# Kernel optimization log

Hardware: AMD Instinct MI355X
Metric: run time of the kernel (lower is better)

The kernel has to match this reference:

```python
import jax, jax.numpy as jnp
from jax import lax
import numpy as np

# ---- model dims ----
VOCAB, DMODEL, NLAYER = 32000, 1024, 4
NHEAD, HEAD = 16, 64              # RWKV6 heads (DMODEL = NHEAD*HEAD)
DIN = 2 * DMODEL                  # mamba expand=2
MHEAD, MHD = DIN // 64, 64        # mamba heads / head_dim (hard-coded 64 in block)
DSTATE, KCONV = 64, 4             # mamba2 state size / depthwise conv kernel
FFH = 4 * DMODEL
B, T = 1, 1024
EPS = 1e-6


def rmsnorm(v, w):
    return w * v * lax.rsqrt(jnp.mean(v * v, axis=-1, keepdims=True) + EPS)


def causal_dwconv(x, w):
    # x: [B,T,C], w: [C,K] depthwise causal conv
    C, K = w.shape
    xp = jnp.pad(x, ((0, 0), (K - 1, 0), (0, 0)))
    return lax.conv_general_dilated(
        xp, w.T[:, None, :], (1,), 'VALID',
        dimension_numbers=('NWC', 'WIO', 'NWC'), feature_group_count=C)


def setup_inputs() -> dict:
    key = jax.random.key(0)
    ks = iter(jax.random.split(key, 64))
    nrm = lambda shape, s=0.02: jax.random.normal(next(ks), shape, jnp.float32) * s
    x = jax.random.randint(next(ks), (B, T), 0, VOCAB)
    inp = dict(
        x=x,
        embed=nrm((VOCAB, DMODEL)),
        ln_w=jnp.ones((NLAYER, DMODEL), jnp.float32),
        Wr=nrm((NLAYER, DMODEL, DMODEL)), Wk=nrm((NLAYER, DMODEL, DMODEL)),
        Wv=nrm((NLAYER, DMODEL, DMODEL)), Ww=nrm((NLAYER, DMODEL, DMODEL)),
        w_bias=nrm((NLAYER, DMODEL), 0.5), u=nrm((NLAYER, NHEAD, HEAD), 0.5),
        Wg=nrm((NLAYER, DMODEL, DMODEL)), Wo=nrm((NLAYER, DMODEL, DMODEL)),
        Win=nrm((NLAYER, DMODEL, 2 * DIN + 2 * DSTATE + MHEAD)),
        conv_w=nrm((NLAYER, DIN + 2 * DSTATE, KCONV), 0.2),
        dt_bias=nrm((NLAYER, MHEAD), 0.5), A_log=nrm((NLAYER, MHEAD), 0.5),
        Dskip=nrm((NLAYER, MHEAD), 0.5),
        mnorm_w=jnp.ones((NLAYER, DIN), jnp.float32),
        Wout_m=nrm((NLAYER, DIN, DMODEL)),
        gate_w=nrm((NLAYER, 2 * DMODEL)), gate_b=jnp.zeros((NLAYER,), jnp.float32),
        ffn_ln_w=jnp.ones((NLAYER, DMODEL), jnp.float32),
        W1=nrm((NLAYER, DMODEL, FFH)), W2=nrm((NLAYER, FFH, DMODEL)),
        ln_out_w=jnp.ones((DMODEL,), jnp.float32),
    )
    return inp


def _block(h, p):
    (p_ln, pWr, pWk, pWv, pWw, p_wb, p_u, pWg, pWo, pWin, p_cw, p_dtb,
     p_Al, p_D, p_mn, pWom, p_gw, p_gb, p_fln, pW1, pW2) = p
    nx = rmsnorm(h, p_ln)

    # ---- RWKV6 linear attention ----
    r = (nx @ pWr).reshape(B, T, NHEAD, HEAD)
    k = (nx @ pWk).reshape(B, T, NHEAD, HEAD)
    v = (nx @ pWv).reshape(B, T, NHEAD, HEAD)
    dec = jnp.exp(-jnp.exp(nx @ pWw + p_wb)).reshape(B, T, NHEAD, HEAD)  # data-dep decay in (0,1)
    g = jax.nn.silu(nx @ pWg)

    def rstep(S, inp):
        rt, kt, vt, dt_ = inp                      # [B,H,hd]
        kv = kt[..., None] * vt[..., None, :]      # [B,H,hd,hd]
        o = jnp.einsum('bhk,bhkv->bhv', rt, S + p_u[None, :, :, None] * kv)
        return dt_[..., None] * S + kv, o

    S0 = jnp.zeros((B, NHEAD, HEAD, HEAD), nx.dtype)
    tmaj = lambda a: jnp.moveaxis(a, 1, 0)
    _, o = lax.scan(rstep, S0, (tmaj(r), tmaj(k), tmaj(v), tmaj(dec)))
    o = jnp.moveaxis(o, 0, 1).reshape(B, T, DMODEL)
    out_rwkv = (o * g) @ pWo

    # ---- Mamba2 selective scan ----
    zxbcdt = nx @ pWin
    z = zxbcdt[..., :DIN]
    xBC = zxbcdt[..., DIN:2 * DIN + 2 * DSTATE]
    dt = zxbcdt[..., -MHEAD:]
    xBC = jax.nn.silu(causal_dwconv(xBC, p_cw))
    xm = xBC[..., :DIN].reshape(B, T, MHEAD, MHD)
    Bm = xBC[..., DIN:DIN + DSTATE]
    Cm = xBC[..., DIN + DSTATE:]
    dt = jax.nn.softplus(dt + p_dtb)               # [B,T,MH]
    dA = jnp.exp(-dt * jnp.exp(p_Al))              # [B,T,MH]

    def mstep(hst, inp):
        xt, Bt, Ct, dAt, dtt = inp                 # [B,MH,hd],[B,ds],[B,ds],[B,MH],[B,MH]
        hst = dAt[..., None, None] * hst + (dtt[..., None] * xt)[..., None] * Bt[:, None, None, :]
        y = jnp.einsum('bhps,bs->bhp', hst, Ct)
        return hst, y

    h0 = jnp.zeros((B, MHEAD, MHD, DSTATE), nx.dtype)
    _, ym = lax.scan(mstep, h0, (tmaj(xm), tmaj(Bm), tmaj(Cm), tmaj(dA), tmaj(dt)))
    ym = jnp.moveaxis(ym, 0, 1) + p_D[None, None, :, None] * xm
    ym = ym.reshape(B, T, DIN)
    ym = rmsnorm(ym * jax.nn.silu(z), p_mn)        # gated RMSNorm
    out_mamba = ym @ pWom

    # ---- gated fusion + residual + FFN ----
    cat = jnp.concatenate([out_rwkv, out_mamba], axis=-1)
    gate = jax.nn.sigmoid(jnp.einsum('btd,d->bt', cat, p_gw) + p_gb)[..., None]
    h = h + gate * out_rwkv + (1.0 - gate) * out_mamba
    h = h + jax.nn.gelu(rmsnorm(h, p_fln) @ pW1, approximate=False) @ pW2
    return h


def reference(x, embed, ln_w, Wr, Wk, Wv, Ww, w_bias, u, Wg, Wo, Win, conv_w,
              dt_bias, A_log, Dskip, mnorm_w, Wout_m, gate_w, gate_b,
              ffn_ln_w, W1, W2, ln_out_w):
    h = embed[x]  # [B,T,D]
    params = (ln_w, Wr, Wk, Wv, Ww, w_bias, u, Wg, Wo, Win, conv_w, dt_bias,
              A_log, Dskip, mnorm_w, Wout_m, gate_w, gate_b, ffn_ln_w, W1, W2)
    h, _ = lax.scan(lambda c, p: (_block(c, p), None), h, params)
    logits = rmsnorm(h, ln_out_w) @ embed.T  # tied head
    return logits
```

## Files before the change

### kernel.cpp

```cpp
#include <hip/hip_runtime.h>
#include <hip/hip_bf16.h>
#include <math.h>

#define T 1024
#define NLAYER 4
#define NHEAD 16
#define HEAD 64
#define DIN 2048
#define MHEAD 32
#define DSTATE 64
#define FFH 4096
#define NWIN 4256
#define CCONV 2176
#define VOCABSZ 32000
#define NCHUNK 16
#define PKROWS 9472
#define PKN 9376

typedef unsigned short u16;
typedef __attribute__((ext_vector_type(8))) short s16x8;
typedef __attribute__((ext_vector_type(4))) float f32x4;

__device__ inline u16 f2bf(float f) {
  union { float f; unsigned u; } v; v.f = f;
  return (u16)((v.u + 0x7FFF + ((v.u >> 16) & 1)) >> 16);
}
__device__ inline float bf2f(u16 s) {
  union { unsigned u; float f; } v; v.u = ((unsigned)s) << 16;
  return v.f;
}
__device__ inline float sigf(float x) { return 1.f / (1.f + expf(-x)); }

__device__ inline void gload16(const void* g, void* l) {
  __builtin_amdgcn_global_load_lds(
      (__attribute__((address_space(1))) void*)(size_t)g,
      (__attribute__((address_space(3))) void*)(unsigned int)(size_t)l,
      16, 0, 0);
}

#define SWZ_SRC(lane) ((((lane) & 7) ^ ((lane) >> 3)) * 8)
#define SWZ_RD(kb, lk8, rsw) (((((kb) + (lk8)) >> 3) ^ (rsw)) << 3)

__device__ inline float block_sum(float v, float* sb) {
  #pragma unroll
  for (int o = 32; o; o >>= 1) v += __shfl_down(v, o);
  int w = threadIdx.x >> 6;
  if ((threadIdx.x & 63) == 0) sb[w] = v;
  __syncthreads();
  float s = sb[0] + sb[1] + sb[2] + sb[3];
  __syncthreads();
  return s;
}

__global__ __launch_bounds__(256) void k_cast(const float* __restrict__ s, u16* __restrict__ d) {
  size_t i = ((size_t)blockIdx.x * 256 + threadIdx.x) * 4;
  float4 v = *(const float4*)&s[i];
  u16 o[4] = {f2bf(v.x), f2bf(v.y), f2bf(v.z), f2bf(v.w)};
  *(uint2*)&d[i] = *(uint2*)o;
}

__global__ __launch_bounds__(256) void k_tcast(const float* __restrict__ src, size_t sstride,
                                               u16* __restrict__ dst, size_t dstride,
                                               int K, int N) {
  __shared__ float S[64][65];
  const float* sp = src + (size_t)blockIdx.z * sstride;
  u16* dp = dst + (size_t)blockIdx.z * dstride;
  int n0 = blockIdx.x * 64, k0 = blockIdx.y * 64;
  int tid = threadIdx.x;
  int tr = tid >> 4, tc = (tid & 15) * 4;
  #pragma unroll
  for (int it = 0; it < 4; ++it) {
    int r = tr + it * 16;
    int col = n0 + tc;
    float4 v;
    if (col + 3 < N) v = *(const float4*)&sp[(size_t)(k0 + r) * N + col];
    else {
      v.x = (col + 0 < N) ? sp[(size_t)(k0 + r) * N + col + 0] : 0.f;
      v.y = (col + 1 < N) ? sp[(size_t)(k0 + r) * N + col + 1] : 0.f;
      v.z = (col + 2 < N) ? sp[(size_t)(k0 + r) * N + col + 2] : 0.f;
      v.w = 0.f;
    }
    S[r][tc + 0] = v.x; S[r][tc + 1] = v.y; S[r][tc + 2] = v.z; S[r][tc + 3] = v.w;
  }
  __syncthreads();
  #pragma unroll
  for (int it = 0; it < 4; ++it) {
    int rn = tr + it * 16;
    if (n0 + rn >= N) continue;
    u16 o[4];
    o[0] = f2bf(S[tc + 0][rn]); o[1] = f2bf(S[tc + 1][rn]);
    o[2] = f2bf(S[tc + 2][rn]); o[3] = f2bf(S[tc + 3][rn]);
    *(uint2*)&dp[(size_t)(n0 + rn) * K + k0 + tc] = *(uint2*)o;
  }
}

struct TC6 { const float* src[6]; u16* dst[6]; size_t dstride[6]; };
__global__ __launch_bounds__(256) void k_tcast6(TC6 tc) {
  __shared__ float S[64][65];
  int w = blockIdx.z >> 2, l = blockIdx.z & 3;
  const float* sp = tc.src[w] + (size_t)l * 1024 * 1024;
  u16* dp = tc.dst[w] + (size_t)l * tc.dstride[w];
  int n0 = blockIdx.x * 64, k0 = blockIdx.y * 64;
  int tid = threadIdx.x;
  int tr = tid >> 4, tcc = (tid & 15) * 4;
  #pragma unroll
  for (int it = 0; it < 4; ++it) {
    int r = tr + it * 16;
    float4 v = *(const float4*)&sp[(size_t)(k0 + r) * 1024 + n0 + tcc];
    S[r][tcc + 0] = v.x; S[r][tcc + 1] = v.y; S[r][tcc + 2] = v.z; S[r][tcc + 3] = v.w;
  }
  __syncthreads();
  #pragma unroll
  for (int it = 0; it < 4; ++it) {
    int rn = tr + it * 16;
    u16 o[4];
    o[0] = f2bf(S[tcc + 0][rn]); o[1] = f2bf(S[tcc + 1][rn]);
    o[2] = f2bf(S[tcc + 2][rn]); o[3] = f2bf(S[tcc + 3][rn]);
    *(uint2*)&dp[(size_t)(n0 + rn) * 1024 + k0 + tcc] = *(uint2*)o;
  }
}

__global__ __launch_bounds__(256) void k_embln(const int* x, const float* embed,
                                               const float* w, float* h, u16* out) {
  __shared__ float sb[8];
  int t = blockIdx.x, tid = threadIdx.x;
  int row = x[t];
  float4 v = *(const float4*)&embed[(size_t)row * 1024 + tid * 4];
  *(float4*)&h[(size_t)t * 1024 + tid * 4] = v;
  float ss = v.x * v.x + v.y * v.y + v.z * v.z + v.w * v.w;
  float tot = block_sum(ss, sb);
  float rn = rsqrtf(tot / 1024.f + 1e-6f);
  int c = tid * 4;
  u16 o[4] = {f2bf(v.x * rn * w[c + 0]), f2bf(v.y * rn * w[c + 1]),
              f2bf(v.z * rn * w[c + 2]), f2bf(v.w * rn * w[c + 3])};
  *(uint2*)&out[(size_t)t * 1024 + c] = *(uint2*)o;
}

enum { EPI_F32 = 0, EPI_QKV = 1, EPI_GELU = 2 };

struct GOut {
  void* out;
  const float* aux;
  size_t zstride;
  float *r, *k, *v, *ld, *g, *zx;
};

template <int EPI, int BM, int BN, int TH>
__global__ __launch_bounds__(TH) void k_gemm2(const u16* __restrict__ A,
                                              const u16* __restrict__ Bt,
                                              int N, int K, int kLen, GOut go) {
  union SmemG {
    u16 st[2][BM + BN][64];
    float cb[BM][BN];
  };
  __shared__ __align__(16) SmemG sm;
  constexpr int NW = TH / 64;
  constexpr int NWM = (NW == 8) ? 4 : 2;
  constexpr int NWN = NW / NWM;
  constexpr int FR = BM / NWM / 16, FC = BN / NWN / 16;
  constexpr int ROWS = BM + BN;
  constexpr int RPW = ROWS / NW;
  constexpr int LPS = RPW / 8;
  int tid = threadIdx.x, lane = tid & 63, wid = tid >> 6;
  int lid = blockIdx.y * gridDim.x + blockIdx.x;
  int nwg = gridDim.x * gridDim.y;
  int q = nwg >> 3, r8 = nwg & 7;
  int xcd = lid & 7, pos = lid >> 3;
  int wg = (xcd < r8) ? (xcd * (q + 1) + pos) : (r8 * (q + 1) + (xcd - r8) * q + pos);
  int m0 = (wg % gridDim.x) * BM, n0 = (wg / gridDim.x) * BN;
  int kOff = blockIdx.z * kLen;
  int wr = (wid / NWN) * (BM / NWM), wc = (wid % NWN) * (BN / NWN);
  int lr = lane & 15, lk8 = (lane >> 4) * 8;
  int rsw = lr & 7;
  int swc = SWZ_SRC(lane);
  int rA = lane >> 3;
  f32x4 acc[FR][FC] = {};

  auto STAGE = [&](int buf, int k0) {
    #pragma unroll
    for (int it = 0; it < LPS; ++it) {
      int rb = wid * RPW + it * 8;
      if (rb < BM)
        gload16(&A[(size_t)(m0 + rb + rA) * K + k0 + swc], &sm.st[buf][rb][0]);
      else
        gload16(&Bt[(size_t)(n0 + rb - BM + rA) * K + k0 + swc], &sm.st[buf][rb][0]);
    }
  };
  auto COMPUTE = [&](int buf) {
    #pragma unroll
    for (int kb = 0; kb < 64; kb += 32) {
      s16x8 af[FR], bf[FC];
      #pragma unroll
      for (int i = 0; i < FR; ++i)
        af[i] = *(const s16x8*)&sm.st[buf][wr + i * 16 + lr][SWZ_RD(kb, lk8, rsw)];
      #pragma unroll
      for (int j = 0; j < FC; ++j)
        bf[j] = *(const s16x8*)&sm.st[buf][BM + wc + j * 16 + lr][SWZ_RD(kb, lk8, rsw)];
      #pragma unroll
      for (int i = 0; i < FR; ++i)
        #pragma unroll
        for (int j = 0; j < FC; ++j)
          acc[i][j] = __builtin_amdgcn_mfma_f32_16x16x32_bf16(af[i], bf[j], acc[i][j], 0, 0, 0);
    }
  };

  int nt = kLen >> 6;
  STAGE(0, kOff);
  int cur = 0;
  for (int t = 0; t < nt; ++t) {
    if (t + 1 < nt) {
      STAGE(cur ^ 1, kOff + (t + 1) * 64);
      asm volatile("s_waitcnt vmcnt(%0)" :: "n"(LPS) : "memory");
    } else {
      asm volatile("s_waitcnt vmcnt(0)" ::: "memory");
    }
    __builtin_amdgcn_s_barrier();
    __builtin_amdgcn_sched_barrier(0);
    COMPUTE(cur);
    __builtin_amdgcn_s_barrier();
    cur ^= 1;
  }

  if constexpr (EPI == EPI_F32) {
    float* outf = (float*)go.out + (size_t)blockIdx.z * go.zstride;
    #pragma unroll
    for (int i = 0; i < FR; ++i)
      #pragma unroll
      for (int j = 0; j < FC; ++j) {
        int row = m0 + wr + i * 16 + ((lane >> 4) << 2);
        int col = n0 + wc + j * 16 + lr;
        if (col >= N) continue;
        #pragma unroll
        for (int r_ = 0; r_ < 4; ++r_)
          outf[(size_t)(row + r_) * N + col] = acc[i][j][r_];
      }
  } else {
    __syncthreads();
    #pragma unroll
    for (int i = 0; i < FR; ++i)
      #pragma unroll
      for (int j = 0; j < FC; ++j) {
        int rrow = wr + i * 16 + ((lane >> 4) << 2);
        int ccol = wc + j * 16 + lr;
        #pragma unroll
        for (int r_ = 0; r_ < 4; ++r_)
          sm.cb[rrow + r_][ccol] = acc[i][j][r_];
      }
    __syncthreads();
    constexpr int RPB = BN / 4;
    constexpr int ITERS = (BM * RPB) / TH;
    if constexpr (EPI == EPI_GELU) {
      u16* outb = (u16*)go.out;
      #pragma unroll
      for (int it2 = 0; it2 < ITERS; ++it2) {
        int idx = it2 * TH + tid;
        int row = idx / RPB, c4 = (idx % RPB) * 4;
        int gc = n0 + c4;
        if (gc + 3 >= N) continue;
        float4 v = *(const float4*)&sm.cb[row][c4];
        u16 o[4];
        o[0] = f2bf(0.5f * v.x * (1.f + erff(v.x * 0.70710678118654752f)));
        o[1] = f2bf(0.5f * v.y * (1.f + erff(v.y * 0.70710678118654752f)));
        o[2] = f2bf(0.5f * v.z * (1.f + erff(v.z * 0.70710678118654752f)));
        o[3] = f2bf(0.5f * v.w * (1.f + erff(v.w * 0.70710678118654752f)));
        *(uint2*)&outb[(size_t)(m0 + row) * N + gc] = *(uint2*)o;
      }
    } else {
      float* tptr; int ldbw, coff, op;
      if (n0 < 5120) {
        int tsel = n0 >> 10;
        tptr = (tsel == 0) ? go.r : (tsel == 1) ? go.k : (tsel == 2) ? go.v
             : (tsel == 3) ? go.ld : go.g;
        ldbw = 1024; coff = n0 & 1023;
        op = (tsel == 3) ? 1 : (tsel == 4) ? 2 : 0;
      } else {
        tptr = go.zx; ldbw = 4256; coff = n0 - 5120; op = 0;
      }
      #pragma unroll
      for (int it2 = 0; it2 < ITERS; ++it2) {
        int idx = it2 * TH + tid;
        int row = idx / RPB, c4 = (idx % RPB) * 4;
        int gc = n0 + c4;
        if (gc >= N) continue;
        float4 v = *(const float4*)&sm.cb[row][c4];
        float* pv = (float*)&v;
        if (op == 1) {
          #pragma unroll
          for (int e = 0; e < 4; ++e) pv[e] = -__expf(pv[e] + go.aux[coff + c4 + e]);
        } else if (op == 2) {
          #pragma unroll
          for (int e = 0; e < 4; ++e) pv[e] = pv[e] * sigf(pv[e]);
        }
        if (gc + 3 < N) *(float4*)&tptr[(size_t)(m0 + row) * ldbw + coff + c4] = v;
        else {
          for (int e = 0; e < 4 && gc + e < N; ++e)
            tptr[(size_t)(m0 + row) * ldbw + coff + c4 + e] = pv[e];
        }
      }
    }
  }
}

struct DualArg {
  const u16 *A0, *A1, *B0, *B1;
  float *o0, *o1;
  int K0, K1;
};
__global__ __launch_bounds__(256) void k_dual(DualArg da) {
  union SmemD {
    u16 st[2][128][64];
    float cb[64][64];
  };
  __shared__ __align__(16) SmemD sm;
  const u16* A  = blockIdx.z ? da.A1 : da.A0;
  const u16* Bt = blockIdx.z ? da.B1 : da.B0;
  float* out    = blockIdx.z ? da.o1 : da.o0;
  int K         = blockIdx.z ? da.K1 : da.K0;
  const int N = 1024;
  int tid = threadIdx.x, lane = tid & 63, wid = tid >> 6;
  int lid = blockIdx.y * gridDim.x + blockIdx.x;
  int nwg = gridDim.x * gridDim.y;
  int q = nwg >> 3, r8 = nwg & 7;
  int xcd = lid & 7, pos = lid >> 3;
  int wg = (xcd < r8) ? (xcd * (q + 1) + pos) : (r8 * (q + 1) + (xcd - r8) * q + pos);
  int m0 = (wg % gridDim.x) * 64, n0 = (wg / gridDim.x) * 64;
  int wr = (wid >> 1) * 32, wc = (wid & 1) * 32;
  int lr = lane & 15, lk8 = (lane >> 4) * 8;
  int rsw = lr & 7, swc = SWZ_SRC(lane), rA = lane >> 3;
  f32x4 acc[2][2] = {};
  auto STAGE = [&](int buf, int k0) {
    #pragma unroll
    for (int it = 0; it < 2; ++it) {
      int rb = wid * 16 + it * 8;
      gload16(&A[(size_t)(m0 + rb + rA) * K + k0 + swc], &sm.st[buf][rb][0]);
      gload16(&Bt[(size_t)(n0 + rb + rA) * K + k0 + swc], &sm.st[buf][64 + rb][0]);
    }
  };
  auto COMPUTE = [&](int buf) {
    #pragma unroll
    for (int kb = 0; kb < 64; kb += 32) {
      s16x8 af[2], bf[2];
      #pragma unroll
      for (int i = 0; i < 2; ++i)
        af[i] = *(const s16x8*)&sm.st[buf][wr + i * 16 + lr][SWZ_RD(kb, lk8, rsw)];
      #pragma unroll
      for (int j = 0; j < 2; ++j)
        bf[j] = *(const s16x8*)&sm.st[buf][64 + wc + j * 16 + lr][SWZ_RD(kb, lk8, rsw)];
      #pragma unroll
      for (int i = 0; i < 2; ++i)
        #pragma unroll
        for (int j = 0; j < 2; ++j)
          acc[i][j] = __builtin_amdgcn_mfma_f32_16x16x32_bf16(af[i], bf[j], acc[i][j], 0, 0, 0);
    }
  };
  int nt = K >> 6;
  STAGE(0, 0);
  int cur = 0;
  for (int t = 0; t < nt; ++t) {
    if (t + 1 < nt) {
      STAGE(cur ^ 1, (t + 1) * 64);
      asm volatile("s_waitcnt vmcnt(4)" ::: "memory");
    } else {
      asm volatile("s_waitcnt vmcnt(0)" ::: "memory");
    }
    __builtin_amdgcn_s_barrier();
    __builtin_amdgcn_sched_barrier(0);
    COMPUTE(cur);
    __builtin_amdgcn_s_barrier();
    cur ^= 1;
  }
  __syncthreads();
  #pragma unroll
  for (int i = 0; i < 2; ++i)
    #pragma unroll
    for (int j = 0; j < 2; ++j) {
      int rrow = wr + i * 16 + ((lane >> 4) << 2);
      int ccol = wc + j * 16 + lr;
      #pragma unroll
      for (int r_ = 0; r_ < 4; ++r_)
        sm.cb[rrow + r_][ccol] = acc[i][j][r_];
    }
  __syncthreads();
  #pragma unroll
  for (int it2 = 0; it2 < 4; ++it2) {
    int idx = it2 * 256 + tid;
    int row = idx >> 4, c4 = (idx & 15) * 4;
    *(float4*)&out[(size_t)(m0 + row) * N + n0 + c4] = *(const float4*)&sm.cb[row][c4];
  }
}

__global__ __launch_bounds__(256) void k_conv(const float* __restrict__ zx,
                                              const float* __restrict__ cw,
                                              float* __restrict__ xc) {
  int c = (blockIdx.x * 256 + threadIdx.x) * 4;
  int t = blockIdx.y;
  if (c >= CCONV) return;
  float4 w0 = *(const float4*)&cw[(c + 0) * 4];
  float4 w1 = *(const float4*)&cw[(c + 1) * 4];
  float4 w2 = *(const float4*)&cw[(c + 2) * 4];
  float4 w3 = *(const float4*)&cw[(c + 3) * 4];
  float4 a = {0.f, 0.f, 0.f, 0.f};
  #pragma unroll
  for (int tap = 0; tap < 4; ++tap) {
    int tt = t - 3 + tap;
    if (tt < 0) continue;
    float4 z = *(const float4*)&zx[(size_t)tt * NWIN + 2048 + c];
    a.x += z.x * ((const float*)&w0)[tap];
    a.y += z.y * ((const float*)&w1)[tap];
    a.z += z.z * ((const float*)&w2)[tap];
    a.w += z.w * ((const float*)&w3)[tap];
  }
  a.x = a.x * sigf(a.x); a.y = a.y * sigf(a.y);
  a.z = a.z * sigf(a.z); a.w = a.w * sigf(a.w);
  *(float4*)&xc[(size_t)t * CCONV + c] = a;
}

__global__ __launch_bounds__(256) void k_dtbc(const float* __restrict__ zx,
                                              const float* __restrict__ xc,
                                              const float* __restrict__ dt_bias,
                                              const float* __restrict__ A_log,
                                              float* __restrict__ dtb, float* __restrict__ la,
                                              float* __restrict__ BC) {
  int c = blockIdx.x, tid = threadIdx.x;
  if (blockIdx.y == 0) {
    __shared__ float ldaS[64][33];
    #pragma unroll
    for (int it = 0; it < 8; ++it) {
      int e = it * 256 + tid;
      int i = e >> 5, j = e & 31;
      float x = zx[(size_t)(c * 64 + i) * NWIN + 4224 + j] + dt_bias[j];
      float sp = (x > 20.f) ? x : log1pf(expf(x));
      dtb[(size_t)(c * 64 + i) * 32 + j] = sp;
      ldaS[i][j] = -sp * expf(A_log[j]);
    }
    __syncthreads();
    if (tid < 32) {
      float g = 0.f;
      for (int i = 0; i < 64; ++i) {
        g += ldaS[i][tid];
        la[((size_t)c * 32 + tid) * 64 + i] = g;
      }
    }
  } else {
    __shared__ float Bc[64][65];
    __shared__ float Cc[16][65];
    int i0 = (blockIdx.y - 1) * 16;
    #pragma unroll
    for (int it = 0; it < 4; ++it) {
      int idx = it * 256 + tid;
      int r = idx >> 4, c4 = (idx & 15) * 4;
      float4 b4 = *(const float4*)&xc[(size_t)(c * 64 + r) * CCONV + 2048 + c4];
      Bc[r][c4] = b4.x; Bc[r][c4+1] = b4.y; Bc[r][c4+2] = b4.z; Bc[r][c4+3] = b4.w;
    }
    {
      int r = tid >> 4, c4 = (tid & 15) * 4;
      float4 cv = *(const float4*)&xc[(size_t)(c * 64 + i0 + r) * CCONV + 2112 + c4];
      Cc[r][c4] = cv.x; Cc[r][c4+1] = cv.y; Cc[r][c4+2] = cv.z; Cc[r][c4+3] = cv.w;
    }
    __syncthreads();
    int il = tid >> 4, sg = tid & 15;
    float acc[4] = {};
    for (int d = 0; d < 64; ++d) {
      float cv = Cc[il][d];
      #pragma unroll
      for (int j = 0; j < 4; ++j) acc[j] += Bc[sg * 4 + j][d] * cv;
    }
    #pragma unroll
    for (int j = 0; j < 4; ++j)
      BC[((size_t)c * 64 + i0 + il) * 64 + sg * 4 + j] = acc[j];
  }
}

union SmemH1 {
  struct { float rS[64][66], kS[64][66], gS[64][66]; u16 khS[64][64]; u16 vtS[64][72]; float uS[64]; } a;
  struct { u16 XT[64][72], BT[64][72]; float fS[64]; } b;
};
__global__ __launch_bounds__(256) void k_heads1(const float* __restrict__ rbuf,
                                                const float* __restrict__ kbuf,
                                                const float* __restrict__ ldbuf,
                                                const float* __restrict__ vbuf,
                                                const float* __restrict__ u,
                                                const float* __restrict__ xc,
                                                const float* __restrict__ la,
                                                const float* __restrict__ dtb,
                                                u16* __restrict__ rt, float* __restrict__ eL,
                                                u16* __restrict__ G, float* __restrict__ U,
                                                float* __restrict__ Um) {
  __shared__ SmemH1 sm;
  int c = blockIdx.x, tid = threadIdx.x;
  int lane = tid & 63, wid = tid >> 6;
  int lr = lane & 15, lk8 = (lane >> 4) * 8, rsw = lr & 7;
  int wr = (wid >> 1) * 32, wc = (wid & 1) * 32;
  if (blockIdx.y < 16) {
    int h = blockIdx.y;
    #pragma unroll
    for (int it = 0; it < 4; ++it) {
      int idx = it * 256 + tid;
      int i = idx >> 4, c4 = (idx & 15) * 4;
      size_t base = (size_t)(c * 64 + i) * 1024 + h * 64 + c4;
      float4 rv = *(const float4*)&rbuf[base];
      float4 kv = *(const float4*)&kbuf[base];
      float4 lv = *(const float4*)&ldbuf[base];
      float4 vv = *(const float4*)&vbuf[base];
      sm.a.rS[i][c4] = rv.x; sm.a.rS[i][c4+1] = rv.y; sm.a.rS[i][c4+2] = rv.z; sm.a.rS[i][c4+3] = rv.w;
      sm.a.kS[i][c4] = kv.x; sm.a.kS[i][c4+1] = kv.y; sm.a.kS[i][c4+2] = kv.z; sm.a.kS[i][c4+3] = kv.w;
      sm.a.gS[i][c4] = lv.x; sm.a.gS[i][c4+1] = lv.y; sm.a.gS[i][c4+2] = lv.z; sm.a.gS[i][c4+3] = lv.w;
      sm.a.vtS[c4 + 0][i] = f2bf(vv.x); sm.a.vtS[c4 + 1][i] = f2bf(vv.y);
      sm.a.vtS[c4 + 2][i] = f2bf(vv.z); sm.a.vtS[c4 + 3][i] = f2bf(vv.w);
    }
    if (tid < 64) sm.a.uS[tid] = u[h * 64 + tid];
    __syncthreads();
    if (tid < 64) {
      int k = tid;
      float g = 0.f;
      for (int i = 0; i < 64; ++i) {
        float ld = sm.a.gS[i][k];
        sm.a.gS[i][k] = g;
        rt[(size_t)(c * 64 + i) * 1024 + h * 64 + k] = f2bf(sm.a.rS[i][k] * __expf(g));
        g += ld;
      }
      float gL = g;
      eL[((size_t)c * 16 + h) * 64 + k] = __expf(gL);
      for (int i = 0; i < 64; ++i) {
        float gincl = (i < 63) ? sm.a.gS[i + 1][k] : gL;
        int col = (((i >> 3) ^ (k & 7)) << 3) | (i & 7);
        sm.a.khS[k][col] = f2bf(sm.a.kS[i][k] * __expf(fminf(gL - gincl, 0.f)));
      }
    }
    __syncthreads();
    {
      int i = tid & 63, sg = tid >> 6;
      float acc[16] = {};
      float accd = 0.f;
      for (int k = 0; k < 64; ++k) {
        float rv = sm.a.rS[i][k], gi = sm.a.gS[i][k];
        accd += rv * sm.a.uS[k] * sm.a.kS[i][k];
        #pragma unroll
        for (int j = 0; j < 16; ++j) {
          int s = sg * 16 + j;
          int sp1 = (s < 63) ? s + 1 : 63;
          acc[j] += rv * sm.a.kS[s][k] * __expf(fminf(gi - sm.a.gS[sp1][k], 0.f));
        }
      }
      #pragma unroll
      for (int j = 0; j < 16; ++j) {
        int s = sg * 16 + j;
        float v = (s < i) ? acc[j] : ((s == i) ? accd : 0.f);
        G[(((size_t)c * 16 + h) * 64 + i) * 64 + s] = f2bf(v);
      }
    }
    {
      size_t gb = ((size_t)c * 16 + h) * 64;
      f32x4 acc2[2][2] = {};
      #pragma unroll
      for (int kb = 0; kb < 64; kb += 32) {
        s16x8 a[2], b[2];
        #pragma unroll
        for (int i_ = 0; i_ < 2; ++i_)
          a[i_] = *(const s16x8*)&sm.a.khS[wr + i_ * 16 + lr][SWZ_RD(kb, lk8, rsw)];
        #pragma unroll
        for (int j_ = 0; j_ < 2; ++j_)
          b[j_] = *(const s16x8*)&sm.a.vtS[wc + j_ * 16 + lr][kb + lk8];
        #pragma unroll
        for (int i_ = 0; i_ < 2; ++i_)
          #pragma unroll
          for (int j_ = 0; j_ < 2; ++j_)
            acc2[i_][j_] = __builtin_amdgcn_mfma_f32_16x16x32_bf16(a[i_], b[j_], acc2[i_][j_], 0, 0, 0);
      }
      #pragma unroll
      for (int i_ = 0; i_ < 2; ++i_)
        #pragma unroll
        for (int j_ = 0; j_ < 2; ++j_) {
          int row = wr + i_ * 16 + ((lane >> 4) << 2);
          int col = wc + j_ * 16 + lr;
          #pragma unroll
          for (int r_ = 0; r_ < 4; ++r_)
            U[(gb + row + r_) * 64 + col] = acc2[i_][j_][r_];
        }
    }
  } else {
    int h = blockIdx.y - 16;
    size_t lb = ((size_t)c * 32 + h) * 64;
    if (tid < 64) {
      float la63 = la[lb + 63];
      sm.b.fS[tid] = dtb[(size_t)(c * 64 + tid) * 32 + h] * __expf(fminf(la63 - la[lb + tid], 0.f));
    }
    __syncthreads();
    #pragma unroll
    for (int it = 0; it < 4; ++it) {
      int idx = it * 256 + tid;
      int t = idx >> 4, p4 = (idx & 15) * 4;
      float f = sm.b.fS[t];
      float4 xv = *(const float4*)&xc[(size_t)(c * 64 + t) * CCONV + h * 64 + p4];
      sm.b.XT[p4 + 0][t] = f2bf(f * xv.x); sm.b.XT[p4 + 1][t] = f2bf(f * xv.y);
      sm.b.XT[p4 + 2][t] = f2bf(f * xv.z); sm.b.XT[p4 + 3][t] = f2bf(f * xv.w);
      float4 bv = *(const float4*)&xc[(size_t)(c * 64 + t) * CCONV + 2048 + p4];
      sm.b.BT[p4 + 0][t] = f2bf(bv.x); sm.b.BT[p4 + 1][t] = f2bf(bv.y);
      sm.b.BT[p4 + 2][t] = f2bf(bv.z); sm.b.BT[p4 + 3][t] = f2bf(bv.w);
    }
    __syncthreads();
    f32x4 acc[2][2] = {};
    #pragma unroll
    for (int kb = 0; kb < 64; kb += 32) {
      s16x8 a[2], b[2];
      #pragma unroll
      for (int i = 0; i < 2; ++i) a[i] = *(const s16x8*)&sm.b.XT[wr + i * 16 + lr][kb + lk8];
      #pragma unroll
      for (int j = 0; j < 2; ++j) b[j] = *(const s16x8*)&sm.b.BT[wc + j * 16 + lr][kb + lk8];
      #pragma unroll
      for (int i = 0; i < 2; ++i)
        #pragma unroll
        for (int j = 0; j < 2; ++j)
          acc[i][j] = __builtin_amdgcn_mfma_f32_16x16x32_bf16(a[i], b[j], acc[i][j], 0, 0, 0);
    }
    #pragma unroll
    for (int i = 0; i < 2; ++i)
      #pragma unroll
      for (int j = 0; j < 2; ++j) {
        int row = wr + i * 16 + ((lane >> 4) << 2);
        int col = wc + j * 16 + lr;
        #pragma unroll
        for (int r_ = 0; r_ < 4; ++r_)
          Um[(lb + row + r_) * 64 + col] = acc[i][j][r_];
      }
  }
}

__global__ __launch_bounds__(256) void k_scan2(const float* __restrict__ Urw,
                                               const float* __restrict__ eL,
                                               u16* __restrict__ Sall,
                                               const float* __restrict__ Um,
                                               const float* __restrict__ la,
                                               u16* __restrict__ hall) {
  int tid = threadIdx.x;
  if (blockIdx.x < 16) {
    int h = blockIdx.x;
    int k = tid >> 2, v0 = blockIdx.y * 16 + (tid & 3) * 4;
    float S[4] = {};
    for (int c = 0; c < 16; ++c) {
      size_t gb = ((size_t)c * 16 + h) * 64;
      u16 tmp[4] = {f2bf(S[0]), f2bf(S[1]), f2bf(S[2]), f2bf(S[3])};
      *(uint2*)&Sall[(gb + k) * 64 + v0] = *(uint2*)&tmp[0];
      float e = eL[gb + k];
      float4 uv = *(const float4*)&Urw[(gb + k) * 64 + v0];
      S[0] = e * S[0] + uv.x; S[1] = e * S[1] + uv.y;
      S[2] = e * S[2] + uv.z; S[3] = e * S[3] + uv.w;
    }
  } else {
    int h = blockIdx.x - 16;
    int p = tid >> 2, s0 = blockIdx.y * 16 + (tid & 3) * 4;
    float S[4] = {};
    for (int c = 0; c < 16; ++c) {
      size_t lb = ((size_t)c * 32 + h) * 64;
      u16 tmp[4] = {f2bf(S[0]), f2bf(S[1]), f2bf(S[2]), f2bf(S[3])};
      *(uint2*)&hall[(lb + p) * 64 + s0] = *(uint2*)&tmp[0];
      float e = __expf(la[lb + 63]);
      float4 uv = *(const float4*)&Um[(lb + p) * 64 + s0];
      S[0] = e * S[0] + uv.x; S[1] = e * S[1] + uv.y;
      S[2] = e * S[2] + uv.z; S[3] = e * S[3] + uv.w;
    }
  }
}

union SmemH2 {
  struct { u16 rtS[64][64], GS[64][64], StS[64][72], vtS[64][72]; } a;
  struct { u16 MS[64][64], hS[64][64], CtS[64][72], XT2[64][72]; float laS[64], dtbS[64], eS[64]; } b;
};
__global__ __launch_bounds__(256) void k_heads2(const u16* __restrict__ rt,
                                                const u16* __restrict__ Gb,
                                                const u16* __restrict__ Sall,
                                                const float* __restrict__ vbuf,
                                                const float* __restrict__ gbuf,
                                                u16* __restrict__ og,
                                                const u16* __restrict__ hall,
                                                const float* __restrict__ xc,
                                                const float* __restrict__ la,
                                                const float* __restrict__ dtb,
                                                const float* __restrict__ BC,
                                                float* __restrict__ ymb) {
  __shared__ SmemH2 sm;
  int c = blockIdx.x, tid = threadIdx.x;
  int lane = tid & 63, wid = tid >> 6;
  int lr = lane & 15, lk8 = (lane >> 4) * 8;
  int rsw = lr & 7, swc = SWZ_SRC(lane);
  int wr = (wid >> 1) * 32, wc = (wid & 1) * 32;
  if (blockIdx.y < 16) {
    int h = blockIdx.y;
    size_t gb = ((size_t)c * 16 + h) * 64;
    #pragma unroll
    for (int it = 0; it < 2; ++it) {
      int rb = wid * 16 + it * 8;
      int r = rb + (lane >> 3);
      gload16(&rt[(size_t)(c * 64 + r) * 1024 + h * 64 + swc], &sm.a.rtS[rb][0]);
      gload16(&Gb[(gb + r) * 64 + swc], &sm.a.GS[rb][0]);
    }
    #pragma unroll
    for (int it = 0; it < 2; ++it) {
      int idx = it * 256 + tid;
      int k = idx >> 3, c8 = (idx & 7) * 8;
      uint4 ld = *(const uint4*)&Sall[(gb + k) * 64 + c8];
      const u16* pv = (const u16*)&ld;
      #pragma unroll
      for (int jj = 0; jj < 8; ++jj) sm.a.StS[c8 + jj][k] = pv[jj];
    }
    #pragma unroll
    for (int it = 0; it < 4; ++it) {
      int idx = it * 256 + tid;
      int s = idx >> 4, v4 = (idx & 15) * 4;
      float4 vv = *(const float4*)&vbuf[(size_t)(c * 64 + s) * 1024 + h * 64 + v4];
      sm.a.vtS[v4 + 0][s] = f2bf(vv.x); sm.a.vtS[v4 + 1][s] = f2bf(vv.y);
      sm.a.vtS[v4 + 2][s] = f2bf(vv.z); sm.a.vtS[v4 + 3][s] = f2bf(vv.w);
    }
    __syncthreads();
    f32x4 acc[2][2] = {};
    #pragma unroll
    for (int kb = 0; kb < 64; kb += 32) {
      s16x8 aR[2], aG[2], bS[2], bV[2];
      #pragma unroll
      for (int i = 0; i < 2; ++i) {
        aR[i] = *(const s16x8*)&sm.a.rtS[wr + i * 16 + lr][SWZ_RD(kb, lk8, rsw)];
        aG[i] = *(const s16x8*)&sm.a.GS[wr + i * 16 + lr][SWZ_RD(kb, lk8, rsw)];
      }
      #pragma unroll
      for (int j = 0; j < 2; ++j) {
        bS[j] = *(const s16x8*)&sm.a.StS[wc + j * 16 + lr][kb + lk8];
        bV[j] = *(const s16x8*)&sm.a.vtS[wc + j * 16 + lr][kb + lk8];
      }
      #pragma unroll
      for (int i = 0; i < 2; ++i)
        #pragma unroll
        for (int j = 0; j < 2; ++j) {
          acc[i][j] = __builtin_amdgcn_mfma_f32_16x16x32_bf16(aR[i], bS[j], acc[i][j], 0, 0, 0);
          acc[i][j] = __builtin_amdgcn_mfma_f32_16x16x32_bf16(aG[i], bV[j], acc[i][j], 0, 0, 0);
        }
    }
    #pragma unroll
    for (int i = 0; i < 2; ++i)
      #pragma unroll
      for (int j = 0; j < 2; ++j) {
        int row = c * 64 + wr + i * 16 + ((lane >> 4) << 2);
        int col = h * 64 + wc + j * 16 + lr;
        #pragma unroll
        for (int r_ = 0; r_ < 4; ++r_) {
          size_t idx = (size_t)(row + r_) * 1024 + col;
          og[idx] = f2bf(acc[i][j][r_] * gbuf[idx]);
        }
      }
  } else {
    int h = blockIdx.y - 16;
    size_t lb = ((size_t)c * 32 + h) * 64;
    if (tid < 64) {
      float lv = la[lb + tid];
      sm.b.laS[tid] = lv;
      sm.b.eS[tid] = __expf(lv);
      sm.b.dtbS[tid] = dtb[(size_t)(c * 64 + tid) * 32 + h];
    }
    #pragma unroll
    for (int it = 0; it < 2; ++it) {
      int rb = wid * 16 + it * 8;
      int r = rb + (lane >> 3);
      gload16(&hall[(lb + r) * 64 + swc], &sm.b.hS[rb][0]);
    }
    __syncthreads();
    #pragma unroll
    for (int it = 0; it < 4; ++it) {
      int idx = it * 256 + tid;
      int i = idx >> 4, s4 = (idx & 15) * 4;
      float lai = sm.b.laS[i];
      float4 bc4 = *(const float4*)&BC[((size_t)c * 64 + i) * 64 + s4];
      u16 mo[4];
      #pragma unroll
      for (int j = 0; j < 4; ++j) {
        int s = s4 + j;
        float bcv = (j == 0) ? bc4.x : (j == 1) ? bc4.y : (j == 2) ? bc4.z : bc4.w;
        float v = 0.f;
        if (s <= i)
          v = __expf(fminf(lai - sm.b.laS[s], 0.f)) * sm.b.dtbS[s] * bcv;
        mo[j] = f2bf(v);
      }
      *(uint2*)&sm.b.MS[i][(((s4 >> 3) ^ (i & 7)) << 3) | (s4 & 7)] = *(uint2*)mo;
      float ei = sm.b.eS[i];
      float4 cv = *(const float4*)&xc[(size_t)(c * 64 + i) * CCONV + 2112 + s4];
      sm.b.CtS[i][s4 + 0] = f2bf(ei * cv.x); sm.b.CtS[i][s4 + 1] = f2bf(ei * cv.y);
      sm.b.CtS[i][s4 + 2] = f2bf(ei * cv.z); sm.b.CtS[i][s4 + 3] = f2bf(ei * cv.w);
      float4 xv = *(const float4*)&xc[(size_t)(c * 64 + i) * CCONV + h * 64 + s4];
      sm.b.XT2[s4 + 0][i] = f2bf(xv.x); sm.b.XT2[s4 + 1][i] = f2bf(xv.y);
      sm.b.XT2[s4 + 2][i] = f2bf(xv.z); sm.b.XT2[s4 + 3][i] = f2bf(xv.w);
    }
    __syncthreads();
    f32x4 acc[2][2] = {};
    #pragma unroll
    for (int kb = 0; kb < 64; kb += 32) {
      s16x8 aM[2], aC[2], bX[2], bH[2];
      #pragma unroll
      for (int i = 0; i < 2; ++i) {
        aM[i] = *(const s16x8*)&sm.b.MS[wr + i * 16 + lr][SWZ_RD(kb, lk8, rsw)];
        aC[i] = *(const s16x8*)&sm.b.CtS[wr + i * 16 + lr][kb + lk8];
      }
      #pragma unroll
      for (int j = 0; j < 2; ++j) {
        bX[j] = *(const s16x8*)&sm.b.XT2[wc + j * 16 + lr][kb + lk8];
        bH[j] = *(const s16x8*)&sm.b.hS[wc + j * 16 + lr][SWZ_RD(kb, lk8, rsw)];
      }
      #pragma unroll
      for (int i = 0; i < 2; ++i)
        #pragma unroll
        for (int j = 0; j < 2; ++j) {
          acc[i][j] = __builtin_amdgcn_mfma_f32_16x16x32_bf16(aM[i], bX[j], acc[i][j], 0, 0, 0);
          acc[i][j] = __builtin_amdgcn_mfma_f32_16x16x32_bf16(aC[i], bH[j], acc[i][j], 0, 0, 0);
        }
    }
    #pragma unroll
    for (int i = 0; i < 2; ++i)
      #pragma unroll
      for (int j = 0; j < 2; ++j) {
        int row = c * 64 + wr + i * 16 + ((lane >> 4) << 2);
        int col = h * 64 + wc + j * 16 + lr;
        #pragma unroll
        for (int r_ = 0; r_ < 4; ++r_)
          ymb[(size_t)(row + r_) * 2048 + col] = acc[i][j][r_];
      }
  }
}

__global__ __launch_bounds__(256) void k_ymn(const float* ymb, const float* xc,
                                             const float* zx, const float* Dsk,
                                             const float* mnw, u16* out) {
  __shared__ float sb[8];
  int t = blockIdx.x, tid = threadIdx.x;
  float vals[8];
  float ss = 0.f;
  #pragma unroll
  for (int j = 0; j < 8; ++j) {
    int cidx = j * 256 + tid;
    float yv = ymb[(size_t)t * 2048 + cidx] + Dsk[cidx >> 6] * xc[(size_t)t * CCONV + cidx];
    float zv = zx[(size_t)t * NWIN + cidx];
    float val = yv * zv * sigf(zv);
    vals[j] = val;
    ss += val * val;
  }
  float tot = block_sum(ss, sb);
  float rn = rsqrtf(tot / 2048.f + 1e-6f);
  #pragma unroll
  for (int j = 0; j < 8; ++j) {
    int cidx = j * 256 + tid;
    out[(size_t)t * 2048 + cidx] = f2bf(vals[j] * rn * mnw[cidx]);
  }
}

__global__ __launch_bounds__(256) void k_gateln(const float* rw, const float* mb,
                                                const float* gw, const float* gb,
                                                float* h, const float* w, u16* nx) {
  __shared__ float sb[8];
  int t = blockIdx.x, tid = threadIdx.x;
  float s = 0.f;
  #pragma unroll
  for (int j = 0; j < 4; ++j) {
    int d = j * 256 + tid;
    s += rw[(size_t)t * 1024 + d] * gw[d] + mb[(size_t)t * 1024 + d] * gw[1024 + d];
  }
  float tot = block_sum(s, sb);
  float gate = sigf(tot + gb[0]);
  float hv[4], ss = 0.f;
  #pragma unroll
  for (int j = 0; j < 4; ++j) {
    int d = j * 256 + tid;
    float v = h[(size_t)t * 1024 + d] + gate * rw[(size_t)t * 1024 + d] +
              (1.f - gate) * mb[(size_t)t * 1024 + d];
    h[(size_t)t * 1024 + d] = v;
    hv[j] = v;
    ss += v * v;
  }
  float tot2 = block_sum(ss, sb);
  float rn = rsqrtf(tot2 / 1024.f + 1e-6f);
  #pragma unroll
  for (int j = 0; j < 4; ++j) {
    int d = j * 256 + tid;
    nx[(size_t)t * 1024 + d] = f2bf(hv[j] * rn * w[d]);
  }
}

__global__ __launch_bounds__(256) void k_redln(const float* __restrict__ part,
                                               float* __restrict__ h,
                                               const float* __restrict__ w,
                                               u16* __restrict__ nx) {
  __shared__ float sb[8];
  int t = blockIdx.x, tid = threadIdx.x;
  size_t base = (size_t)t * 1024 + tid * 4;
  float4 s = *(const float4*)&part[base];
  #pragma unroll
  for (int p = 1; p < 4; ++p) {
    float4 v = *(const float4*)&part[(size_t)p * 1024 * 1024 + base];
    s.x += v.x; s.y += v.y; s.z += v.z; s.w += v.w;
  }
  float4 d = *(const float4*)&h[base];
  s.x += d.x; s.y += d.y; s.z += d.z; s.w += d.w;
  *(float4*)&h[base] = s;
  float ss = s.x * s.x + s.y * s.y + s.z * s.z + s.w * s.w;
  float tot = block_sum(ss, sb);
  float rn = rsqrtf(tot / 1024.f + 1e-6f);
  int c = tid * 4;
  u16 o[4] = {f2bf(s.x * rn * w[c + 0]), f2bf(s.y * rn * w[c + 1]),
              f2bf(s.z * rn * w[c + 2]), f2bf(s.w * rn * w[c + 3])};
  *(uint2*)&nx[(size_t)t * 1024 + c] = *(uint2*)o;
}

extern "C" void kernel_launch(void* const* d_in, const int* in_sizes, int n_in,
                              void* d_out, int out_size, void* d_ws, size_t ws_size,
                              hipStream_t stream) {
  const int*   x       = (const int*)d_in[0];
  const float* embed   = (const float*)d_in[1];
  const float* ln_w    = (const float*)d_in[2];
  const float* Wr      = (const float*)d_in[3];
  const float* Wk      = (const float*)d_in[4];
  const float* Wv      = (const float*)d_in[5];
  const float* Ww      = (const float*)d_in[6];
  const float* w_bias  = (const float*)d_in[7];
  const float* u       = (const float*)d_in[8];
  const float* Wg      = (const float*)d_in[9];
  const float* Wo      = (const float*)d_in[10];
  const float* Win     = (const float*)d_in[11];
  const float* conv_w  = (const float*)d_in[12];
  const float* dt_bias = (const float*)d_in[13];
  const float* A_log   = (const float*)d_in[14];
  const float* Dskip   = (const float*)d_in[15];
  const float* mnorm_w = (const float*)d_in[16];
  const float* Wout_m  = (const float*)d_in[17];
  const float* gate_w  = (const float*)d_in[18];
  const float* gate_b  = (const float*)d_in[19];
  const float* ffn_ln  = (const float*)d_in[20];
  const float* W1      = (const float*)d_in[21];
  const float* W2      = (const float*)d_in[22];
  const float* ln_out  = (const float*)d_in[23];

  char* p = (char*)d_ws;
  auto alloc = [&](size_t bytes) {
    char* r = p;
    p += (bytes + 255) & ~(size_t)255;
    return r;
  };
  u16* embB = (u16*)alloc((size_t)VOCABSZ * 1024 * 2);
  u16* Wpk  = (u16*)alloc((size_t)NLAYER * PKROWS * 1024 * 2);
  u16* WoT  = (u16*)alloc((size_t)NLAYER * 1024 * 1024 * 2);
  u16* WomT = (u16*)alloc((size_t)NLAYER * 1024 * 2048 * 2);
  u16* W1T  = (u16*)alloc((size_t)NLAYER * 4096 * 1024 * 2);
  u16* W2T  = (u16*)alloc((size_t)NLAYER * 1024 * 4096 * 2);
  float* h        = (float*)alloc((size_t)T * 1024 * 4);
  u16*   nx       = (u16*)alloc((size_t)T * 1024 * 2);
  float* rbuf     = (float*)alloc((size_t)T * 1024 * 4);
  float* kbuf     = (float*)alloc((size_t)T * 1024 * 4);
  float* vbuf     = (float*)alloc((size_t)T * 1024 * 4);
  float* ldbuf    = (float*)alloc((size_t)T * 1024 * 4);
  float* gbuf     = (float*)alloc((size_t)T * 1024 * 4);
  float* zx       = (float*)alloc((size_t)T * NWIN * 4);
  u16*   rt       = (u16*)alloc((size_t)T * 1024 * 2);
  float* eL       = (float*)alloc((size_t)NCHUNK * 16 * 64 * 4);
  u16*   Gb       = (u16*)alloc((size_t)NCHUNK * 16 * 64 * 64 * 2);
  float* Urw      = (float*)alloc((size_t)NCHUNK * 16 * 64 * 64 * 4);
  u16*   Sall     = (u16*)alloc((size_t)NCHUNK * 16 * 64 * 64 * 2);
  u16*   og       = (u16*)alloc((size_t)T * 1024 * 2);
  float* out_rwkv = (float*)alloc((size_t)T * 1024 * 4);
  float* xc       = (float*)alloc((size_t)T * CCONV * 4);
  float* dtb      = (float*)alloc((size_t)T * 32 * 4);
  float* la       = (float*)alloc((size_t)NCHUNK * 32 * 64 * 4);
  float* BC       = (float*)alloc((size_t)NCHUNK * 64 * 64 * 4);
  float* Um       = (float*)alloc((size_t)NCHUNK * 32 * 64 * 64 * 4);
  u16*   hall     = (u16*)alloc((size_t)NCHUNK * 32 * 64 * 64 * 2);
  float* ymb      = (float*)alloc((size_t)T * 2048 * 4);
  u16*   ymn      = (u16*)alloc((size_t)T * 2048 * 2);
  float* out_mam  = (float*)alloc((size_t)T * 1024 * 4);
  u16*   ffa      = (u16*)alloc((size_t)T * FFH * 2);
  float* part     = (float*)alloc((size_t)4 * 1024 * 1024 * 4);

  const size_t PKS = (size_t)PKROWS * 1024;

  k_cast<<<VOCABSZ * 1024 / 1024, 256, 0, stream>>>(embed, embB);
  {
    TC6 tc;
    tc.src[0] = Wr; tc.src[1] = Wk; tc.src[2] = Wv; tc.src[3] = Ww; tc.src[4] = Wg; tc.src[5] = Wo;
    tc.dst[0] = Wpk;               tc.dstride[0] = PKS;
    tc.dst[1] = Wpk + 1024 * 1024; tc.dstride[1] = PKS;
    tc.dst[2] = Wpk + 2048 * 1024; tc.dstride[2] = PKS;
    tc.dst[3] = Wpk + 3072 * 1024; tc.dstride[3] = PKS;
    tc.dst[4] = Wpk + 4096 * 1024; tc.dstride[4] = PKS;
    tc.dst[5] = WoT;               tc.dstride[5] = (size_t)1024 * 1024;
    k_tcast6<<<dim3(16, 16, 24), 256, 0, stream>>>(tc);
  }
  k_tcast<<<dim3(67, 16, 4), 256, 0, stream>>>(Win, (size_t)1024 * NWIN, Wpk + (size_t)5120 * 1024, PKS, 1024, NWIN);
  k_tcast<<<dim3(16, 32, 4), 256, 0, stream>>>(Wout_m, (size_t)2048 * 1024, WomT, (size_t)1024 * 2048, 2048, 1024);
  k_tcast<<<dim3(64, 16, 4), 256, 0, stream>>>(W1, (size_t)1024 * 4096, W1T, (size_t)4096 * 1024, 1024, 4096);
  k_tcast<<<dim3(16, 64, 4), 256, 0, stream>>>(W2, (size_t)4096 * 1024, W2T, (size_t)1024 * 4096, 4096, 1024);

  k_embln<<<1024, 256, 0, stream>>>(x, embed, ln_w, h, nx);

  for (int l = 0; l < NLAYER; ++l) {
    {
      GOut go = {};
      go.r = rbuf; go.k = kbuf; go.v = vbuf; go.ld = ldbuf; go.g = gbuf; go.zx = zx;
      go.aux = w_bias + l * 1024;
      k_gemm2<EPI_QKV, 128, 128, 512><<<dim3(8, 74), 512, 0, stream>>>(nx, Wpk + (size_t)l * PKS, PKN, 1024, 1024, go);
    }
    k_conv<<<dim3(3, 1024), 256, 0, stream>>>(zx, conv_w + (size_t)l * CCONV * 4, xc);
    k_dtbc<<<dim3(16, 5), 256, 0, stream>>>(zx, xc, dt_bias + l * 32, A_log + l * 32, dtb, la, BC);
    k_heads1<<<dim3(16, 48), 256, 0, stream>>>(rbuf, kbuf, ldbuf, vbuf, u + (size_t)l * 1024,
                                               xc, la, dtb, rt, eL, Gb, Urw, Um);
    k_scan2<<<dim3(48, 4), 256, 0, stream>>>(Urw, eL, Sall, Um, la, hall);
    k_heads2<<<dim3(16, 48), 256, 0, stream>>>(rt, Gb, Sall, vbuf, gbuf, og,
                                               hall, xc, la, dtb, BC, ymb);
    k_ymn<<<1024, 256, 0, stream>>>(ymb, xc, zx, Dskip + l * 32, mnorm_w + (size_t)l * 2048, ymn);
    {
      DualArg da;
      da.A0 = og;  da.B0 = WoT + (size_t)l * 1024 * 1024;  da.o0 = out_rwkv; da.K0 = 1024;
      da.A1 = ymn; da.B1 = WomT + (size_t)l * 1024 * 2048; da.o1 = out_mam;  da.K1 = 2048;
      k_dual<<<dim3(16, 16, 2), 256, 0, stream>>>(da);
    }
    k_gateln<<<1024, 256, 0, stream>>>(out_rwkv, out_mam, gate_w + (size_t)l * 2048,
                                       gate_b + l, h, ffn_ln + l * 1024, nx);
    {
      GOut go = {}; go.out = ffa;
      k_gemm2<EPI_GELU, 128, 128, 512><<<dim3(8, 32), 512, 0, stream>>>(nx, W1T + (size_t)l * 4096 * 1024, 4096, 1024, 1024, go);
    }
    {
      GOut go = {}; go.out = part; go.zstride = (size_t)1024 * 1024;
      k_gemm2<EPI_F32, 64, 64, 256><<<dim3(16, 16, 4), 256, 0, stream>>>(ffa, W2T + (size_t)l * 1024 * 4096, 1024, 4096, 1024, go);
    }
    k_redln<<<1024, 256, 0, stream>>>(part, h,
                                      (l < NLAYER - 1) ? (ln_w + (l + 1) * 1024) : ln_out, nx);
  }

  {
    GOut go = {}; go.out = d_out;
    k_gemm2<EPI_F32, 128, 128, 512><<<dim3(8, 250), 512, 0, stream>>>(nx, embB, VOCABSZ, 1024, 1024, go);
  }
}
```

Measured before the change: 1.036 ms.

## Parallelize RWKV cumsum across four waves, store r/k as bf16, halve W2 split-K

The per-chunk decay cumsum in k_heads1 was done by only 64 threads. It now uses all 256 threads through a two-level segmented prefix sum. r and k are staged in shared memory as bf16 instead of fp32, which shrinks LDS use and may improve occupancy, but it adds rounding to the intra-chunk G computation and extra conversion instructions. Separately, the FFN down-projection split-K drops from 4 to 2 slices, with K per slice doubled, so the reduction kernel reads less partial data. The cost is fewer blocks in that GEMM.

```diff
diff --git a/kernel.cpp b/kernel.cpp
--- a/kernel.cpp
+++ b/kernel.cpp
@@ -472,7 +472,9 @@
 }
 
 union SmemH1 {
-  struct { float rS[64][66], kS[64][66], gS[64][66]; u16 khS[64][64]; u16 vtS[64][72]; float uS[64]; } a;
+  struct { u16 rB[64][72], kB[64][72]; float gS[64][66];
+           u16 khS[64][64]; u16 vtS[64][72];
+           float uS[64]; float segsum[4][65]; } a;
   struct { u16 XT[64][72], BT[64][72]; float fS[64]; } b;
 };
 __global__ __launch_bounds__(256) void k_heads1(const float* __restrict__ rbuf,
@@ -502,44 +504,58 @@
       float4 kv = *(const float4*)&kbuf[base];
       float4 lv = *(const float4*)&ldbuf[base];
       float4 vv = *(const float4*)&vbuf[base];
-      sm.a.rS[i][c4] = rv.x; sm.a.rS[i][c4+1] = rv.y; sm.a.rS[i][c4+2] = rv.z; sm.a.rS[i][c4+3] = rv.w;
-      sm.a.kS[i][c4] = kv.x; sm.a.kS[i][c4+1] = kv.y; sm.a.kS[i][c4+2] = kv.z; sm.a.kS[i][c4+3] = kv.w;
-      sm.a.gS[i][c4] = lv.x; sm.a.gS[i][c4+1] = lv.y; sm.a.gS[i][c4+2] = lv.z; sm.a.gS[i][c4+3] = lv.w;
+      sm.a.rB[i][c4+0] = f2bf(rv.x); sm.a.rB[i][c4+1] = f2bf(rv.y);
+      sm.a.rB[i][c4+2] = f2bf(rv.z); sm.a.rB[i][c4+3] = f2bf(rv.w);
+      sm.a.kB[i][c4+0] = f2bf(kv.x); sm.a.kB[i][c4+1] = f2bf(kv.y);
+      sm.a.kB[i][c4+2] = f2bf(kv.z); sm.a.kB[i][c4+3] = f2bf(kv.w);
+      sm.a.gS[i][c4+0] = lv.x; sm.a.gS[i][c4+1] = lv.y;
+      sm.a.gS[i][c4+2] = lv.z; sm.a.gS[i][c4+3] = lv.w;
       sm.a.vtS[c4 + 0][i] = f2bf(vv.x); sm.a.vtS[c4 + 1][i] = f2bf(vv.y);
       sm.a.vtS[c4 + 2][i] = f2bf(vv.z); sm.a.vtS[c4 + 3][i] = f2bf(vv.w);
     }
     if (tid < 64) sm.a.uS[tid] = u[h * 64 + tid];
     __syncthreads();
-    if (tid < 64) {
-      int k = tid;
-      float g = 0.f;
-      for (int i = 0; i < 64; ++i) {
+    {
+      int k = tid & 63, sg = tid >> 6, i0 = sg * 16;
+      float ssum = 0.f;
+      for (int ii = 0; ii < 16; ++ii) ssum += sm.a.gS[i0 + ii][k];
+      sm.a.segsum[sg][k] = ssum;
+      __syncthreads();
+      float base = 0.f;
+      for (int t2 = 0; t2 < sg; ++t2) base += sm.a.segsum[t2][k];
+      float gL = sm.a.segsum[0][k] + sm.a.segsum[1][k] +
+                 sm.a.segsum[2][k] + sm.a.segsum[3][k];
+      float g = base;
+      for (int ii = 0; ii < 16; ++ii) {
+        int i = i0 + ii;
         float ld = sm.a.gS[i][k];
         sm.a.gS[i][k] = g;
-        rt[(size_t)(c * 64 + i) * 1024 + h * 64 + k] = f2bf(sm.a.rS[i][k] * __expf(g));
+        rt[(size_t)(c * 64 + i) * 1024 + h * 64 + k] =
+            f2bf(bf2f(sm.a.rB[i][k]) * __expf(g));
         g += ld;
       }
-      float gL = g;
-      eL[((size_t)c * 16 + h) * 64 + k] = __expf(gL);
-      for (int i = 0; i < 64; ++i) {
+      if (sg == 0) eL[((size_t)c * 16 + h) * 64 + k] = __expf(gL);
+      __syncthreads();
+      for (int ii = 0; ii < 16; ++ii) {
+        int i = i0 + ii;
         float gincl = (i < 63) ? sm.a.gS[i + 1][k] : gL;
         int col = (((i >> 3) ^ (k & 7)) << 3) | (i & 7);
-        sm.a.khS[k][col] = f2bf(sm.a.kS[i][k] * __expf(fminf(gL - gincl, 0.f)));
-      }
-    }
-    __syncthreads();
+        sm.a.khS[k][col] = f2bf(bf2f(sm.a.kB[i][k]) * __expf(fminf(gL - gincl, 0.f)));
+      }
+      __syncthreads();
+    }
     {
       int i = tid & 63, sg = tid >> 6;
       float acc[16] = {};
       float accd = 0.f;
       for (int k = 0; k < 64; ++k) {
-        float rv = sm.a.rS[i][k], gi = sm.a.gS[i][k];
-        accd += rv * sm.a.uS[k] * sm.a.kS[i][k];
+        float rv = bf2f(sm.a.rB[i][k]), gi = sm.a.gS[i][k];
+        accd += rv * sm.a.uS[k] * bf2f(sm.a.kB[i][k]);
         #pragma unroll
         for (int j = 0; j < 16; ++j) {
           int s = sg * 16 + j;
           int sp1 = (s < 63) ? s + 1 : 63;
-          acc[j] += rv * sm.a.kS[s][k] * __expf(fminf(gi - sm.a.gS[sp1][k], 0.f));
+          acc[j] += rv * bf2f(sm.a.kB[s][k]) * __expf(fminf(gi - sm.a.gS[sp1][k], 0.f));
         }
       }
       #pragma unroll
@@ -889,7 +905,7 @@
   size_t base = (size_t)t * 1024 + tid * 4;
   float4 s = *(const float4*)&part[base];
   #pragma unroll
-  for (int p = 1; p < 4; ++p) {
+  for (int p = 1; p < 2; ++p) {
     float4 v = *(const float4*)&part[(size_t)p * 1024 * 1024 + base];
     s.x += v.x; s.y += v.y; s.z += v.z; s.w += v.w;
   }
@@ -1022,7 +1038,7 @@
     }
     {
       GOut go = {}; go.out = part; go.zstride = (size_t)1024 * 1024;
-      k_gemm2<EPI_F32, 64, 64, 256><<<dim3(16, 16, 4), 256, 0, stream>>>(ffa, W2T + (size_t)l * 1024 * 4096, 1024, 4096, 1024, go);
+      k_gemm2<EPI_F32, 64, 64, 256><<<dim3(16, 16, 2), 256, 0, stream>>>(ffa, W2T + (size_t)l * 1024 * 4096, 1024, 4096, 2048, go);
     }
     k_redln<<<1024, 256, 0, stream>>>(part, h,
                                       (l < NLAYER - 1) ? (ln_w + (l + 1) * 1024) : ln_out, nx);
```

Result: no change. 1.046 ms (+1.0%).
